# Optimization experiments

Measured on AMD Instinct MI355X. Metric: run time of the kernel, lower is better.

Reference implementation:

```python
import jax, jax.numpy as jnp
import numpy as np

B, T, CF, D, H, HD, L, HID = 32, 384, 128, 512, 16, 32, 16, 512
EPS = 1e-6

def _make_pe():
    pos = np.arange(T, dtype=np.float32)[:, None]
    div = np.exp(np.arange(0, D, 2, dtype=np.float32) * (-np.log(10000.0) / D))
    pe = np.zeros((T, D), dtype=np.float32)
    pe[:, 0::2] = np.sin(pos * div)
    pe[:, 1::2] = np.cos(pos * div)
    return jnp.asarray(pe)

def setup_inputs() -> dict:
    key = jax.random.key(0)
    ks = jax.random.split(key, 12)
    n = lambda k, shp: jax.random.normal(k, shp, dtype=jnp.float32) * 0.02
    return {
        "index": jax.random.normal(ks[0], (B, T, CF), dtype=jnp.float32),
        "targets": jax.random.normal(ks[1], (B, T, CF), dtype=jnp.float32),
        "W_embed": n(ks[2], (CF, D)), "b_embed": jnp.zeros((D,), jnp.float32),
        "pe": _make_pe(), "learnable_pe": jnp.zeros((T, D), jnp.float32),
        "Wq": n(ks[3], (L, H, D, HD)), "Wk": n(ks[4], (L, H, D, HD)), "Wv": n(ks[5], (L, H, D, HD)),
        "Wproj": n(ks[6], (L, D, D)), "bproj": jnp.zeros((L, D), jnp.float32),
        "ln1_g": jnp.ones((L, D), jnp.float32), "ln1_b": jnp.zeros((L, D), jnp.float32),
        "ln2_g": jnp.ones((L, D), jnp.float32), "ln2_b": jnp.zeros((L, D), jnp.float32),
        "W1": n(ks[7], (L, D, HID)), "b1": jnp.zeros((L, HID), jnp.float32),
        "W2": n(ks[8], (L, HID, D)), "b2": jnp.zeros((L, D), jnp.float32),
        "W_final": n(ks[9], (D, CF)), "b_final": jnp.zeros((CF,), jnp.float32),
    }

def _ln(x, g, b):
    m = jnp.mean(x, axis=-1, keepdims=True)
    v = jnp.mean(jnp.square(x - m), axis=-1, keepdims=True)
    return (x - m) / jnp.sqrt(v + EPS) * g + b

def reference(index, targets, W_embed, b_embed, pe, learnable_pe,
              Wq, Wk, Wv, Wproj, bproj, ln1_g, ln1_b, ln2_g, ln2_b,
              W1, b1, W2, b2, W_final, b_final):
    mask = jnp.tril(jnp.ones((T, T), dtype=bool))
    # NOTE: original scales by 1/sqrt(C) where C = n_embed (input dim), not head_size
    scale = 1.0 / jnp.sqrt(jnp.float32(D))
    x = index @ W_embed + b_embed          # [B,T,D]
    x = x + pe + learnable_pe

    def blk(x, p):
        wq, wk, wv, wp, bp, g1, bl1, g2, bl2, w1, bb1, w2, bb2 = p
        h = _ln(x, g1, bl1)
        q = jnp.einsum('btc,hcd->bhtd', h, wq)
        k = jnp.einsum('btc,hcd->bhtd', h, wk)
        v = jnp.einsum('btc,hcd->bhtd', h, wv)
        s = jnp.einsum('bhtd,bhsd->bhts', q, k) * scale   # [B,H,T,T]
        s = jnp.where(mask, s, -jnp.inf)
        w = jax.nn.softmax(s, axis=-1)
        o = jnp.einsum('bhts,bhsd->bhtd', w, v)
        o = o.transpose(0, 2, 1, 3).reshape(x.shape[0], T, H * HD)
        x = x + o @ wp + bp                                # attn residual (dropout=eval)
        h2 = _ln(x, g2, bl2)
        x = x + jax.nn.relu(h2 @ w1 + bb1) @ w2 + bb2      # FFN residual
        return x, None

    x, _ = jax.lax.scan(blk, x, (Wq, Wk, Wv, Wproj, bproj, ln1_g, ln1_b,
                                 ln2_g, ln2_b, W1, b1, W2, b2))
    logits = x @ W_final + b_final         # [B,T,CF]
    loss = jnp.mean(jnp.square(logits - targets))
    return logits, loss
```

## Files before the change

### kernel.cpp

```cpp
#include <hip/hip_runtime.h>
#include <hip/hip_bf16.h>

#define B_   32
#define T_   384
#define CF_  128
#define D_   512
#define H_   16
#define HD_  32
#define L_   16
#define HID_ 512
#define M_   (B_*T_)

typedef __bf16 bf16x8 __attribute__((ext_vector_type(8)));
typedef float  f32x4  __attribute__((ext_vector_type(4)));

__device__ __forceinline__ float bf2f(unsigned short u){
    unsigned int x = ((unsigned int)u) << 16;
    return __builtin_bit_cast(float, x);
}
__device__ __forceinline__ unsigned short f2bf(float f){
    unsigned int u = __builtin_bit_cast(unsigned int, f);
    u += 0x7FFFu + ((u >> 16) & 1u);
    return (unsigned short)(u >> 16);
}
__device__ __forceinline__ unsigned int cvtpk(float lo, float hi){
    unsigned int r;
    asm("v_cvt_pk_bf16_f32 %0, %1, %2" : "=v"(r) : "v"(lo), "v"(hi));
    return r;
}

typedef const __attribute__((address_space(1))) unsigned int* gas_p;
typedef __attribute__((address_space(3))) unsigned int*       las_p;
__device__ __forceinline__ void gload16(const void* g, void* l){
    __builtin_amdgcn_global_load_lds((gas_p)g, (las_p)l, 16, 0, 0);
}

#define QSCALE 0.06376580687097174f

template<int EPI>
__global__ __launch_bounds__(256) void gemm_k(
    const unsigned short* __restrict__ A,
    const unsigned short* __restrict__ Bt,
    const float* __restrict__ aux0,
    const float* __restrict__ aux1,
    const float* __restrict__ aux2,
    float* __restrict__ fout,
    unsigned short* __restrict__ bout,
    int K)
{
    __shared__ unsigned short lA[2][128*32];
    __shared__ unsigned short lB[2][128*32];

    const int tid  = threadIdx.x;
    const int lane = tid & 63;
    const int w    = tid >> 6;
    const int wm   = w >> 1, wn = w & 1;
    const int li   = lane & 15, ls = lane >> 4;
    const int m0   = blockIdx.x * 128;
    const int n0   = blockIdx.y * 128;
    const int nkt  = K >> 5;

    const int e0 = tid, e1 = tid + 256;
    const int r0 = e0 >> 2, s0 = (e0 & 3) ^ ((r0 >> 1) & 3);
    const int r1 = e1 >> 2, s1 = (e1 & 3) ^ ((r1 >> 1) & 3);
    const unsigned short* gA0 = A  + (size_t)(m0 + r0)*K + s0*8;
    const unsigned short* gA1 = A  + (size_t)(m0 + r1)*K + s1*8;
    const unsigned short* gB0 = Bt + (size_t)(n0 + r0)*K + s0*8;
    const unsigned short* gB1 = Bt + (size_t)(n0 + r1)*K + s1*8;

#define STAGE(c, kt) do{ \
    const int ko_ = (kt)*32; \
    gload16(gA0 + ko_, &lA[c][w*512]); \
    gload16(gA1 + ko_, &lA[c][2048 + w*512]); \
    gload16(gB0 + ko_, &lB[c][w*512]); \
    gload16(gB1 + ko_, &lB[c][2048 + w*512]); \
}while(0)

    f32x4 acc[4][4];
    #pragma unroll
    for (int i=0;i<4;i++)
        #pragma unroll
        for (int j=0;j<4;j++) acc[i][j] = (f32x4){0.f,0.f,0.f,0.f};

    STAGE(0, 0);
    asm volatile("s_waitcnt vmcnt(0)" ::: "memory");
    __syncthreads();

    int cur = 0;
    for (int kt = 0; kt < nkt; ++kt){
        if (kt + 1 < nkt) STAGE(cur^1, kt+1);
        bf16x8 af[4], bf[4];
        #pragma unroll
        for (int f=0; f<4; ++f){
            const int rA = wm*64 + f*16 + li;
            af[f] = *(const bf16x8*)&lA[cur][rA*32 + ((ls ^ ((rA>>1)&3))*8)];
            const int rB = wn*64 + f*16 + li;
            bf[f] = *(const bf16x8*)&lB[cur][rB*32 + ((ls ^ ((rB>>1)&3))*8)];
        }
        #pragma unroll
        for (int i=0;i<4;i++)
            #pragma unroll
            for (int j=0;j<4;j++)
                acc[i][j] = __builtin_amdgcn_mfma_f32_16x16x32_bf16(af[i], bf[j], acc[i][j], 0, 0, 0);
        __syncthreads();
        cur ^= 1;
    }
#undef STAGE

    #pragma unroll
    for (int i=0;i<4;i++){
        #pragma unroll
        for (int j=0;j<4;j++){
            #pragma unroll
            for (int t=0;t<4;t++){
                const int row = m0 + wm*64 + i*16 + ls*4 + t;
                const int col = n0 + wn*64 + j*16 + li;
                const float v = acc[i][j][t];
                if constexpr (EPI == 0){
                    const int tt = row % T_;
                    bout[row*D_ + col] = f2bf(v + aux0[col] + aux1[tt*D_ + col] + aux2[tt*D_ + col]);
                } else if constexpr (EPI == 2){
                    const int idx = row*D_ + col;
                    bout[idx] = f2bf(bf2f(bout[idx]) + v + aux0[col]);
                } else if constexpr (EPI == 3){
                    const float r = v + aux0[col];
                    bout[row*HID_ + col] = f2bf(r > 0.f ? r : 0.f);
                } else {
                    fout[row*CF_ + col] = v + aux0[col];
                }
            }
        }
    }
}

__global__ __launch_bounds__(256) void gemm192_k(
    const unsigned short* __restrict__ A,
    const unsigned short* __restrict__ Bt,
    unsigned short* __restrict__ bout,
    int K)
{
    __shared__ unsigned short lA[2][128*32];
    __shared__ unsigned short lB[2][192*32];

    const int tid  = threadIdx.x;
    const int lane = tid & 63;
    const int w    = tid >> 6;
    const int wm   = w >> 1, wn = w & 1;
    const int li   = lane & 15, ls = lane >> 4;
    const int m0   = blockIdx.x * 128;
    const int n0   = blockIdx.y * 192;
    const int nkt  = K >> 5;

    const int ea0 = tid, ea1 = tid + 256;
    const int ra0 = ea0 >> 2, sa0 = (ea0 & 3) ^ ((ra0 >> 1) & 3);
    const int ra1 = ea1 >> 2, sa1 = (ea1 & 3) ^ ((ra1 >> 1) & 3);
    const unsigned short* gA0 = A + (size_t)(m0 + ra0)*K + sa0*8;
    const unsigned short* gA1 = A + (size_t)(m0 + ra1)*K + sa1*8;

    const int eb0 = tid, eb1 = tid + 256, eb2 = tid + 512;
    const int rb0 = eb0 >> 2, sb0 = (eb0 & 3) ^ ((rb0 >> 1) & 3);
    const int rb1 = eb1 >> 2, sb1 = (eb1 & 3) ^ ((rb1 >> 1) & 3);
    const int rb2 = eb2 >> 2, sb2 = (eb2 & 3) ^ ((rb2 >> 1) & 3);
    const unsigned short* gB0 = Bt + (size_t)(n0 + rb0)*K + sb0*8;
    const unsigned short* gB1 = Bt + (size_t)(n0 + rb1)*K + sb1*8;
    const unsigned short* gB2 = Bt + (size_t)(n0 + rb2)*K + sb2*8;

#define STAGE192(c, kt) do{ \
    const int ko_ = (kt)*32; \
    gload16(gA0 + ko_, &lA[c][w*512]); \
    gload16(gA1 + ko_, &lA[c][2048 + w*512]); \
    gload16(gB0 + ko_, &lB[c][w*512]); \
    gload16(gB1 + ko_, &lB[c][2048 + w*512]); \
    gload16(gB2 + ko_, &lB[c][4096 + w*512]); \
}while(0)

    f32x4 acc[4][6];
    #pragma unroll
    for (int i=0;i<4;i++)
        #pragma unroll
        for (int j=0;j<6;j++) acc[i][j] = (f32x4){0.f,0.f,0.f,0.f};

    STAGE192(0, 0);
    asm volatile("s_waitcnt vmcnt(0)" ::: "memory");
    __syncthreads();

    int cur = 0;
    for (int kt = 0; kt < nkt; ++kt){
        if (kt + 1 < nkt) STAGE192(cur^1, kt+1);
        bf16x8 af[4], bf[6];
        #pragma unroll
        for (int f=0; f<4; ++f){
            const int rA = wm*64 + f*16 + li;
            af[f] = *(const bf16x8*)&lA[cur][rA*32 + ((ls ^ ((rA>>1)&3))*8)];
        }
        #pragma unroll
        for (int f=0; f<6; ++f){
            const int rB = wn*96 + f*16 + li;
            bf[f] = *(const bf16x8*)&lB[cur][rB*32 + ((ls ^ ((rB>>1)&3))*8)];
        }
        #pragma unroll
        for (int i=0;i<4;i++)
            #pragma unroll
            for (int j=0;j<6;j++)
                acc[i][j] = __builtin_amdgcn_mfma_f32_16x16x32_bf16(af[i], bf[j], acc[i][j], 0, 0, 0);
        __syncthreads();
        cur ^= 1;
    }
#undef STAGE192

    #pragma unroll
    for (int i=0;i<4;i++){
        #pragma unroll
        for (int j=0;j<6;j++){
            const int row0 = m0 + wm*64 + i*16 + ls*4;
            const int col  = n0 + wn*96 + j*16 + li;
            const int mat = col >> 9, nl = col & 511;
            const int hh = nl >> 5, dd = nl & 31;
            const int bb = row0 / T_, tt0 = row0 - bb*T_;
            if (mat == 2){
                alignas(8) unsigned short p4[4];
                #pragma unroll
                for (int t=0;t<4;t++) p4[t] = f2bf(acc[i][j][t]);
                *(uint2*)(bout + 2*(size_t)(M_*D_)
                          + ((size_t)(bb*H_ + hh)*HD_ + dd)*T_ + tt0) = *(const uint2*)p4;
            } else {
                #pragma unroll
                for (int t=0;t<4;t++){
                    float v = acc[i][j][t];
                    if (mat == 0) v *= QSCALE;
                    bout[(size_t)mat*(M_*D_)
                         + (((size_t)(bb*H_ + hh)*T_ + tt0 + t)*HD_) + dd] = f2bf(v);
                }
            }
        }
    }
}

__global__ __launch_bounds__(256) void ln_k(const unsigned short* __restrict__ x,
                                            const float* __restrict__ g,
                                            const float* __restrict__ b,
                                            unsigned short* __restrict__ out)
{
    const int w = threadIdx.x >> 6, lane = threadIdx.x & 63;
    const int row = blockIdx.x*4 + w;
    const unsigned short* xr = x + (size_t)row*D_ + lane*8;
    const uint4 raw = *(const uint4*)xr;
    const unsigned short* rs = (const unsigned short*)&raw;
    float v8[8];
    float s = 0.f, q2 = 0.f;
    #pragma unroll
    for (int i=0;i<8;i++){
        v8[i] = bf2f(rs[i]);
        s  += v8[i];
        q2 += v8[i]*v8[i];
    }
    #pragma unroll
    for (int off=32; off; off>>=1){
        s  += __shfl_xor(s,  off);
        q2 += __shfl_xor(q2, off);
    }
    const float mean = s * (1.f/512.f);
    const float var  = q2 * (1.f/512.f) - mean*mean;
    const float rstd = rsqrtf(var + 1e-6f);
    const float4 gA = *(const float4*)(g + lane*8);
    const float4 gB = *(const float4*)(g + lane*8 + 4);
    const float4 bA = *(const float4*)(b + lane*8);
    const float4 bB = *(const float4*)(b + lane*8 + 4);
    alignas(16) unsigned short o8[8];
    o8[0] = f2bf((v8[0]-mean)*rstd*gA.x + bA.x);
    o8[1] = f2bf((v8[1]-mean)*rstd*gA.y + bA.y);
    o8[2] = f2bf((v8[2]-mean)*rstd*gA.z + bA.z);
    o8[3] = f2bf((v8[3]-mean)*rstd*gA.w + bA.w);
    o8[4] = f2bf((v8[4]-mean)*rstd*gB.x + bB.x);
    o8[5] = f2bf((v8[5]-mean)*rstd*gB.y + bB.y);
    o8[6] = f2bf((v8[6]-mean)*rstd*gB.z + bB.z);
    o8[7] = f2bf((v8[7]-mean)*rstd*gB.w + bB.w);
    *(uint4*)(out + (size_t)row*D_ + lane*8) = *(const uint4*)o8;
}

__global__ __launch_bounds__(256) void attn_k(const unsigned short* __restrict__ q,
                                              const unsigned short* __restrict__ k,
                                              const unsigned short* __restrict__ vt,
                                              unsigned short* __restrict__ o)
{
    __shared__ unsigned int Pb[4][2*16*18];

    const int orig = blockIdx.x;
    const int wg   = (orig & 7)*192 + (orig >> 3);
    const int bh   = wg / 3;
    const int t0   = (wg - bh*3) * 128;

    const int tid  = threadIdx.x;
    const int lane = tid & 63, w = tid >> 6;
    const int li   = lane & 15, ls = lane >> 4;
    const unsigned short* qb = q  + (size_t)bh*(T_*HD_);
    const unsigned short* kb = k  + (size_t)bh*(T_*HD_);
    const unsigned short* vb = vt + (size_t)bh*(HD_*T_);

    const int trow0 = t0 + w*32;
    const bf16x8 qaA = *(const bf16x8*)(qb + (trow0 + li)*HD_ + ls*8);
    const bf16x8 qaB = *(const bf16x8*)(qb + (trow0 + 16 + li)*HD_ + ls*8);
    const int nfull = trow0 >> 5;

    float lsA = 0.f, lsB = 0.f;
    f32x4 oA0={0.f,0.f,0.f,0.f}, oA1={0.f,0.f,0.f,0.f};
    f32x4 oB0={0.f,0.f,0.f,0.f}, oB1={0.f,0.f,0.f,0.f};
    unsigned int* pwA = Pb[w];
    unsigned int* pwB = Pb[w] + 288;

    bf16x8 kf0 = *(const bf16x8*)(kb + li*HD_ + ls*8);
    bf16x8 kf1 = *(const bf16x8*)(kb + (16 + li)*HD_ + ls*8);
    bf16x8 vf0 = *(const bf16x8*)(vb + li*T_ + ls*8);
    bf16x8 vf1 = *(const bf16x8*)(vb + (16 + li)*T_ + ls*8);

    for (int c = 0; c < nfull; ++c){
        f32x4 sA0={0.f,0.f,0.f,0.f}, sA1={0.f,0.f,0.f,0.f};
        f32x4 sB0={0.f,0.f,0.f,0.f}, sB1={0.f,0.f,0.f,0.f};
        sA0 = __builtin_amdgcn_mfma_f32_16x16x32_bf16(kf0, qaA, sA0, 0, 0, 0);
        sA1 = __builtin_amdgcn_mfma_f32_16x16x32_bf16(kf1, qaA, sA1, 0, 0, 0);
        sB0 = __builtin_amdgcn_mfma_f32_16x16x32_bf16(kf0, qaB, sB0, 0, 0, 0);
        sB1 = __builtin_amdgcn_mfma_f32_16x16x32_bf16(kf1, qaB, sB1, 0, 0, 0);
        kf0 = *(const bf16x8*)(kb + ((c+1)*32 + li)*HD_ + ls*8);
        kf1 = *(const bf16x8*)(kb + ((c+1)*32 + 16 + li)*HD_ + ls*8);

        float pA0[4], pA1[4], pB0[4], pB1[4];
        #pragma unroll
        for (int j=0;j<4;j++){
            pA0[j] = exp2f(sA0[j]); pA1[j] = exp2f(sA1[j]);
            pB0[j] = exp2f(sB0[j]); pB1[j] = exp2f(sB1[j]);
        }
        lsA += pA0[0]+pA0[1]+pA0[2]+pA0[3]+pA1[0]+pA1[1]+pA1[2]+pA1[3];
        lsB += pB0[0]+pB0[1]+pB0[2]+pB0[3]+pB1[0]+pB1[1]+pB1[2]+pB1[3];

        const uint2 wA0 = { cvtpk(pA0[0], pA0[1]), cvtpk(pA0[2], pA0[3]) };
        const uint2 wA1 = { cvtpk(pA1[0], pA1[1]), cvtpk(pA1[2], pA1[3]) };
        const uint2 wB0 = { cvtpk(pB0[0], pB0[1]), cvtpk(pB0[2], pB0[3]) };
        const uint2 wB1 = { cvtpk(pB1[0], pB1[1]), cvtpk(pB1[2], pB1[3]) };
        *(uint2*)&pwA[li*18 + ls*2]     = wA0;
        *(uint2*)&pwA[li*18 + 8 + ls*2] = wA1;
        *(uint2*)&pwB[li*18 + ls*2]     = wB0;
        *(uint2*)&pwB[li*18 + 8 + ls*2] = wB1;
        asm volatile("s_waitcnt lgkmcnt(0)" ::: "memory");
        const bf16x8 paA = *(const bf16x8*)&pwA[li*18 + ls*4];
        const bf16x8 paB = *(const bf16x8*)&pwB[li*18 + ls*4];

        oA0 = __builtin_amdgcn_mfma_f32_16x16x32_bf16(paA, vf0, oA0, 0, 0, 0);
        oA1 = __builtin_amdgcn_mfma_f32_16x16x32_bf16(paA, vf1, oA1, 0, 0, 0);
        oB0 = __builtin_amdgcn_mfma_f32_16x16x32_bf16(paB, vf0, oB0, 0, 0, 0);
        oB1 = __builtin_amdgcn_mfma_f32_16x16x32_bf16(paB, vf1, oB1, 0, 0, 0);
        vf0 = *(const bf16x8*)(vb + li*T_ + (c+1)*32 + ls*8);
        vf1 = *(const bf16x8*)(vb + (16 + li)*T_ + (c+1)*32 + ls*8);
    }

    {
        f32x4 sA0={0.f,0.f,0.f,0.f}, sB0={0.f,0.f,0.f,0.f}, sB1={0.f,0.f,0.f,0.f};
        sA0 = __builtin_amdgcn_mfma_f32_16x16x32_bf16(kf0, qaA, sA0, 0, 0, 0);
        sB0 = __builtin_amdgcn_mfma_f32_16x16x32_bf16(kf0, qaB, sB0, 0, 0, 0);
        sB1 = __builtin_amdgcn_mfma_f32_16x16x32_bf16(kf1, qaB, sB1, 0, 0, 0);

        const int qA = li, qB = 16 + li;
        float pA0[4], pB0[4], pB1[4];
        #pragma unroll
        for (int j=0;j<4;j++){
            const int k0 = ls*4 + j;
            pA0[j] = (k0 <= qA)      ? exp2f(sA0[j]) : 0.f;
            pB0[j] = exp2f(sB0[j]);
            pB1[j] = (k0 + 16 <= qB) ? exp2f(sB1[j]) : 0.f;
        }
        lsA += pA0[0]+pA0[1]+pA0[2]+pA0[3];
        lsB += pB0[0]+pB0[1]+pB0[2]+pB0[3]+pB1[0]+pB1[1]+pB1[2]+pB1[3];

        const uint2 wA0 = { cvtpk(pA0[0], pA0[1]), cvtpk(pA0[2], pA0[3]) };
        const uint2 wB0 = { cvtpk(pB0[0], pB0[1]), cvtpk(pB0[2], pB0[3]) };
        const uint2 wB1 = { cvtpk(pB1[0], pB1[1]), cvtpk(pB1[2], pB1[3]) };
        const uint2 zz  = { 0u, 0u };
        *(uint2*)&pwA[li*18 + ls*2]     = wA0;
        *(uint2*)&pwA[li*18 + 8 + ls*2] = zz;
        *(uint2*)&pwB[li*18 + ls*2]     = wB0;
        *(uint2*)&pwB[li*18 + 8 + ls*2] = wB1;
        asm volatile("s_waitcnt lgkmcnt(0)" ::: "memory");
        const bf16x8 paA = *(const bf16x8*)&pwA[li*18 + ls*4];
        const bf16x8 paB = *(const bf16x8*)&pwB[li*18 + ls*4];

        oA0 = __builtin_amdgcn_mfma_f32_16x16x32_bf16(paA, vf0, oA0, 0, 0, 0);
        oA1 = __builtin_amdgcn_mfma_f32_16x16x32_bf16(paA, vf1, oA1, 0, 0, 0);
        oB0 = __builtin_amdgcn_mfma_f32_16x16x32_bf16(paB, vf0, oB0, 0, 0, 0);
        oB1 = __builtin_amdgcn_mfma_f32_16x16x32_bf16(paB, vf1, oB1, 0, 0, 0);
    }

    lsA += __shfl_xor(lsA, 16);  lsA += __shfl_xor(lsA, 32);
    lsB += __shfl_xor(lsB, 16);  lsB += __shfl_xor(lsB, 32);

    const int bb = bh >> 4, hh = bh & 15;
    #pragma unroll
    for (int j=0;j<4;j++){
        const float rsA = __shfl(lsA, ls*4 + j);
        const float rsB = __shfl(lsB, ls*4 + j);
        const float iA = 1.f / rsA, iB = 1.f / rsB;
        const int tgA = trow0 + ls*4 + j;
        const int tgB = tgA + 16;
        o[(size_t)(bb*T_ + tgA)*D_ + hh*HD_ + li]      = f2bf(oA0[j]*iA);
        o[(size_t)(bb*T_ + tgA)*D_ + hh*HD_ + 16 + li] = f2bf(oA1[j]*iA);
        o[(size_t)(bb*T_ + tgB)*D_ + hh*HD_ + li]      = f2bf(oB0[j]*iB);
        o[(size_t)(bb*T_ + tgB)*D_ + hh*HD_ + 16 + li] = f2bf(oB1[j]*iB);
    }
}

__global__ __launch_bounds__(256) void packT_k(const float* __restrict__ src,
                                               unsigned short* __restrict__ dst,
                                               int R, int C)
{
    __shared__ unsigned short tile[64][72];
    const int z  = blockIdx.z;
    const float* s = src + (size_t)z*R*C;
    unsigned short* d = dst + (size_t)z*R*C;
    const int c0 = blockIdx.x*64, r0 = blockIdx.y*64;

    for (int it = threadIdx.x; it < 1024; it += 256){
        const int rr  = it >> 4;
        const int cc4 = (it & 15) << 2;
        const float4 v = *(const float4*)(s + (size_t)(r0+rr)*C + c0 + cc4);
        tile[cc4  ][rr] = f2bf(v.x);
        tile[cc4+1][rr] = f2bf(v.y);
        tile[cc4+2][rr] = f2bf(v.z);
        tile[cc4+3][rr] = f2bf(v.w);
    }
    __syncthreads();
    for (int it = threadIdx.x; it < 512; it += 256){
        const int cc = it >> 3;
        const int ch = (it & 7) << 3;
        *(uint4*)(d + (size_t)(c0+cc)*R + r0 + ch) = *(const uint4*)&tile[cc][ch];
    }
}

__global__ __launch_bounds__(256) void pack_qkv_k(const float* __restrict__ Wq,
                                                  const float* __restrict__ Wk,
                                                  const float* __restrict__ Wv,
                                                  unsigned short* __restrict__ dst)
{
    __shared__ unsigned short tile[32][136];
    const int kc  = blockIdx.x;
    const int mat = blockIdx.y >> 4;
    const int h   = blockIdx.y & 15;
    const int l   = blockIdx.z;
    const float* src = ((mat==0) ? Wq : (mat==1) ? Wk : Wv)
                     + ((size_t)(l*H_ + h)*D_ + kc*128)*HD_;

    for (int it = threadIdx.x; it < 1024; it += 256){
        const int rr  = it >> 3;
        const int dd4 = (it & 7) << 2;
        const float4 v = *(const float4*)(src + (size_t)rr*HD_ + dd4);
        tile[dd4  ][rr] = f2bf(v.x);
        tile[dd4+1][rr] = f2bf(v.y);
        tile[dd4+2][rr] = f2bf(v.z);
        tile[dd4+3][rr] = f2bf(v.w);
    }
    __syncthreads();
    unsigned short* dp = dst + (size_t)l*786432 + (size_t)mat*262144 + kc*128;
    for (int it = threadIdx.x; it < 512; it += 256){
        const int dd = it >> 4;
        const int ch = (it & 15) << 3;
        *(uint4*)(dp + (size_t)(h*32 + dd)*512 + ch) = *(const uint4*)&tile[dd][ch];
    }
}

__global__ void cast4_k(const float* __restrict__ src, unsigned short* __restrict__ dst, int total4)
{
    const int i = blockIdx.x*256 + threadIdx.x;
    if (i >= total4) return;
    const float4 vv = ((const float4*)src)[i];
    alignas(8) unsigned short t[4] = { f2bf(vv.x), f2bf(vv.y), f2bf(vv.z), f2bf(vv.w) };
    *(uint2*)(dst + (size_t)i*4) = *(const uint2*)t;
}

__global__ __launch_bounds__(256) void loss1_k(const float* __restrict__ logits,
                                               const float* __restrict__ tgt,
                                               float* __restrict__ part)
{
    float s = 0.f;
    for (int i = blockIdx.x*256 + threadIdx.x; i < M_*CF_; i += 256*1024){
        const float d = logits[i] - tgt[i];
        s += d*d;
    }
    #pragma unroll
    for (int off=32; off; off>>=1) s += __shfl_xor(s, off);
    __shared__ float ws4[4];
    if ((threadIdx.x & 63) == 0) ws4[threadIdx.x >> 6] = s;
    __syncthreads();
    if (threadIdx.x == 0) part[blockIdx.x] = ws4[0]+ws4[1]+ws4[2]+ws4[3];
}

__global__ __launch_bounds__(256) void loss2_k(const float* __restrict__ part,
                                               float* __restrict__ out)
{
    float s = 0.f;
    for (int i = threadIdx.x; i < 1024; i += 256) s += part[i];
    #pragma unroll
    for (int off=32; off; off>>=1) s += __shfl_xor(s, off);
    __shared__ float ws4[4];
    if ((threadIdx.x & 63) == 0) ws4[threadIdx.x >> 6] = s;
    __syncthreads();
    if (threadIdx.x == 0) out[0] = (ws4[0]+ws4[1]+ws4[2]+ws4[3]) * (1.f/(float)(M_*CF_));
}

static constexpr size_t X_OFF     = 0;
static constexpr size_t H_OFF     = 25165824;
static constexpr size_t O_OFF     = 37748736;
static constexpr size_t QKV_OFF   = 50331648;
static constexpr size_t WQKV_OFF  = 88080384;
static constexpr size_t WPROJ_OFF = 113246208;
static constexpr size_t W1_OFF    = 121634816;
static constexpr size_t W2_OFF    = 130023424;
static constexpr size_t WEMB_OFF  = 138412032;
static constexpr size_t WFIN_OFF  = 138543104;
static constexpr size_t PART_OFF  = 138674176;

extern "C" void kernel_launch(void* const* d_in, const int* in_sizes, int n_in,
                              void* d_out, int out_size, void* d_ws, size_t ws_size,
                              hipStream_t stream)
{
    const float* index   = (const float*)d_in[0];
    const float* targets = (const float*)d_in[1];
    const float* W_embed = (const float*)d_in[2];
    const float* b_embed = (const float*)d_in[3];
    const float* pe      = (const float*)d_in[4];
    const float* lpe     = (const float*)d_in[5];
    const float* Wq      = (const float*)d_in[6];
    const float* Wk      = (const float*)d_in[7];
    const float* Wv      = (const float*)d_in[8];
    const float* Wproj   = (const float*)d_in[9];
    const float* bproj   = (const float*)d_in[10];
    const float* ln1g    = (const float*)d_in[11];
    const float* ln1b    = (const float*)d_in[12];
    const float* ln2g    = (const float*)d_in[13];
    const float* ln2b    = (const float*)d_in[14];
    const float* W1      = (const float*)d_in[15];
    const float* b1      = (const float*)d_in[16];
    const float* W2      = (const float*)d_in[17];
    const float* b2      = (const float*)d_in[18];
    const float* Wfin    = (const float*)d_in[19];
    const float* bfin    = (const float*)d_in[20];

    char* ws = (char*)d_ws;
    unsigned short* xb    = (unsigned short*)(ws + X_OFF);
    unsigned short* hbuf  = (unsigned short*)(ws + H_OFF);
    unsigned short* obuf  = (unsigned short*)(ws + O_OFF);
    unsigned short* qkv   = (unsigned short*)(ws + QKV_OFF);
    unsigned short* wqkvp = (unsigned short*)(ws + WQKV_OFF);
    unsigned short* wprojp= (unsigned short*)(ws + WPROJ_OFF);
    unsigned short* w1p   = (unsigned short*)(ws + W1_OFF);
    unsigned short* w2p   = (unsigned short*)(ws + W2_OFF);
    unsigned short* wembp = (unsigned short*)(ws + WEMB_OFF);
    unsigned short* wfinp = (unsigned short*)(ws + WFIN_OFF);
    float*          part  = (float*)(ws + PART_OFF);
    float*          logits= (float*)d_out;

    pack_qkv_k<<<dim3(4,48,16), 256, 0, stream>>>(Wq, Wk, Wv, wqkvp);
    packT_k<<<dim3(8,8,16), 256, 0, stream>>>(Wproj, wprojp, 512, 512);
    packT_k<<<dim3(8,8,16), 256, 0, stream>>>(W1,    w1p,    512, 512);
    packT_k<<<dim3(8,8,16), 256, 0, stream>>>(W2,    w2p,    512, 512);
    packT_k<<<dim3(8,2,1),  256, 0, stream>>>(W_embed, wembp, 128, 512);
    packT_k<<<dim3(2,8,1),  256, 0, stream>>>(Wfin,    wfinp, 512, 128);

    cast4_k<<<1536, 256, 0, stream>>>(index, obuf, 393216);
    gemm_k<0><<<dim3(96,4), 256, 0, stream>>>(obuf, wembp, b_embed, pe, lpe, nullptr, xb, 128);

    for (int l = 0; l < L_; ++l){
        ln_k<<<3072, 256, 0, stream>>>(xb, ln1g + l*512, ln1b + l*512, hbuf);
        gemm192_k<<<dim3(96,8), 256, 0, stream>>>(hbuf, wqkvp + (size_t)l*786432, qkv, 512);
        attn_k<<<1536, 256, 0, stream>>>(qkv, qkv + 6291456, qkv + 2*6291456, obuf);
        gemm_k<2><<<dim3(96,4), 256, 0, stream>>>(obuf, wprojp + (size_t)l*262144,
                                                  bproj + l*512, nullptr, nullptr, nullptr, xb, 512);
        ln_k<<<3072, 256, 0, stream>>>(xb, ln2g + l*512, ln2b + l*512, hbuf);
        gemm_k<3><<<dim3(96,4), 256, 0, stream>>>(hbuf, w1p + (size_t)l*262144,
                                                  b1 + l*512, nullptr, nullptr, nullptr, obuf, 512);
        gemm_k<2><<<dim3(96,4), 256, 0, stream>>>(obuf, w2p + (size_t)l*262144,
                                                  b2 + l*512, nullptr, nullptr, nullptr, xb, 512);
    }

    gemm_k<4><<<dim3(96,1), 256, 0, stream>>>(xb, wfinp, bfin, nullptr, nullptr, logits, nullptr, 512);
    loss1_k<<<1024, 256, 0, stream>>>(logits, targets, part);
    loss2_k<<<1, 256, 0, stream>>>(part, logits + 1572864);
}
```

Before: 1.877 ms.

## Process 64 query rows per wave in attention to reuse K/V fragments

The attention kernel now runs 2 waves per block, each handling 64 query rows (four 16-row groups) instead of 32. Each K and V fragment loaded from global memory therefore feeds twice as many MFMAs, and the diagonal handling is split into two masked tail steps. The cost is more registers per wave and larger per-wave LDS staging. Causal work is also less balanced, since waves whose rows lie further down the sequence run longer loops.

```diff
diff --git a/kernel.cpp b/kernel.cpp
--- a/kernel.cpp
+++ b/kernel.cpp
@@ -278,12 +278,12 @@
     *(uint4*)(out + (size_t)row*D_ + lane*8) = *(const uint4*)o8;
 }
 
-__global__ __launch_bounds__(256) void attn_k(const unsigned short* __restrict__ q,
+__global__ __launch_bounds__(128) void attn_k(const unsigned short* __restrict__ q,
                                               const unsigned short* __restrict__ k,
                                               const unsigned short* __restrict__ vt,
                                               unsigned short* __restrict__ o)
 {
-    __shared__ unsigned int Pb[4][2*16*18];
+    __shared__ unsigned int Pb[2][4*288];
 
     const int orig = blockIdx.x;
     const int wg   = (orig & 7)*192 + (orig >> 3);
@@ -297,16 +297,22 @@
     const unsigned short* kb = k  + (size_t)bh*(T_*HD_);
     const unsigned short* vb = vt + (size_t)bh*(HD_*T_);
 
-    const int trow0 = t0 + w*32;
-    const bf16x8 qaA = *(const bf16x8*)(qb + (trow0 + li)*HD_ + ls*8);
+    const int trow0 = t0 + w*64;
+    const bf16x8 qaA = *(const bf16x8*)(qb + (trow0 +      li)*HD_ + ls*8);
     const bf16x8 qaB = *(const bf16x8*)(qb + (trow0 + 16 + li)*HD_ + ls*8);
+    const bf16x8 qaC = *(const bf16x8*)(qb + (trow0 + 32 + li)*HD_ + ls*8);
+    const bf16x8 qaD = *(const bf16x8*)(qb + (trow0 + 48 + li)*HD_ + ls*8);
     const int nfull = trow0 >> 5;
 
-    float lsA = 0.f, lsB = 0.f;
+    float lsA = 0.f, lsB = 0.f, lsC = 0.f, lsD = 0.f;
     f32x4 oA0={0.f,0.f,0.f,0.f}, oA1={0.f,0.f,0.f,0.f};
     f32x4 oB0={0.f,0.f,0.f,0.f}, oB1={0.f,0.f,0.f,0.f};
+    f32x4 oC0={0.f,0.f,0.f,0.f}, oC1={0.f,0.f,0.f,0.f};
+    f32x4 oD0={0.f,0.f,0.f,0.f}, oD1={0.f,0.f,0.f,0.f};
     unsigned int* pwA = Pb[w];
     unsigned int* pwB = Pb[w] + 288;
+    unsigned int* pwC = Pb[w] + 576;
+    unsigned int* pwD = Pb[w] + 864;
 
     bf16x8 kf0 = *(const bf16x8*)(kb + li*HD_ + ls*8);
     bf16x8 kf1 = *(const bf16x8*)(kb + (16 + li)*HD_ + ls*8);
@@ -316,93 +322,188 @@
     for (int c = 0; c < nfull; ++c){
         f32x4 sA0={0.f,0.f,0.f,0.f}, sA1={0.f,0.f,0.f,0.f};
         f32x4 sB0={0.f,0.f,0.f,0.f}, sB1={0.f,0.f,0.f,0.f};
+        f32x4 sC0={0.f,0.f,0.f,0.f}, sC1={0.f,0.f,0.f,0.f};
+        f32x4 sD0={0.f,0.f,0.f,0.f}, sD1={0.f,0.f,0.f,0.f};
         sA0 = __builtin_amdgcn_mfma_f32_16x16x32_bf16(kf0, qaA, sA0, 0, 0, 0);
         sA1 = __builtin_amdgcn_mfma_f32_16x16x32_bf16(kf1, qaA, sA1, 0, 0, 0);
         sB0 = __builtin_amdgcn_mfma_f32_16x16x32_bf16(kf0, qaB, sB0, 0, 0, 0);
         sB1 = __builtin_amdgcn_mfma_f32_16x16x32_bf16(kf1, qaB, sB1, 0, 0, 0);
+        sC0 = __builtin_amdgcn_mfma_f32_16x16x32_bf16(kf0, qaC, sC0, 0, 0, 0);
+        sC1 = __builtin_amdgcn_mfma_f32_16x16x32_bf16(kf1, qaC, sC1, 0, 0, 0);
+        sD0 = __builtin_amdgcn_mfma_f32_16x16x32_bf16(kf0, qaD, sD0, 0, 0, 0);
+        sD1 = __builtin_amdgcn_mfma_f32_16x16x32_bf16(kf1, qaD, sD1, 0, 0, 0);
         kf0 = *(const bf16x8*)(kb + ((c+1)*32 + li)*HD_ + ls*8);
         kf1 = *(const bf16x8*)(kb + ((c+1)*32 + 16 + li)*HD_ + ls*8);
 
-        float pA0[4], pA1[4], pB0[4], pB1[4];
+        float pA0[4], pA1[4], pB0[4], pB1[4], pC0[4], pC1[4], pD0[4], pD1[4];
         #pragma unroll
         for (int j=0;j<4;j++){
             pA0[j] = exp2f(sA0[j]); pA1[j] = exp2f(sA1[j]);
             pB0[j] = exp2f(sB0[j]); pB1[j] = exp2f(sB1[j]);
+            pC0[j] = exp2f(sC0[j]); pC1[j] = exp2f(sC1[j]);
+            pD0[j] = exp2f(sD0[j]); pD1[j] = exp2f(sD1[j]);
         }
         lsA += pA0[0]+pA0[1]+pA0[2]+pA0[3]+pA1[0]+pA1[1]+pA1[2]+pA1[3];
         lsB += pB0[0]+pB0[1]+pB0[2]+pB0[3]+pB1[0]+pB1[1]+pB1[2]+pB1[3];
+        lsC += pC0[0]+pC0[1]+pC0[2]+pC0[3]+pC1[0]+pC1[1]+pC1[2]+pC1[3];
+        lsD += pD0[0]+pD0[1]+pD0[2]+pD0[3]+pD1[0]+pD1[1]+pD1[2]+pD1[3];
 
         const uint2 wA0 = { cvtpk(pA0[0], pA0[1]), cvtpk(pA0[2], pA0[3]) };
         const uint2 wA1 = { cvtpk(pA1[0], pA1[1]), cvtpk(pA1[2], pA1[3]) };
         const uint2 wB0 = { cvtpk(pB0[0], pB0[1]), cvtpk(pB0[2], pB0[3]) };
         const uint2 wB1 = { cvtpk(pB1[0], pB1[1]), cvtpk(pB1[2], pB1[3]) };
+        const uint2 wC0 = { cvtpk(pC0[0], pC0[1]), cvtpk(pC0[2], pC0[3]) };
+        const uint2 wC1 = { cvtpk(pC1[0], pC1[1]), cvtpk(pC1[2], pC1[3]) };
+        const uint2 wD0 = { cvtpk(pD0[0], pD0[1]), cvtpk(pD0[2], pD0[3]) };
+        const uint2 wD1 = { cvtpk(pD1[0], pD1[1]), cvtpk(pD1[2], pD1[3]) };
         *(uint2*)&pwA[li*18 + ls*2]     = wA0;
         *(uint2*)&pwA[li*18 + 8 + ls*2] = wA1;
         *(uint2*)&pwB[li*18 + ls*2]     = wB0;
         *(uint2*)&pwB[li*18 + 8 + ls*2] = wB1;
+        *(uint2*)&pwC[li*18 + ls*2]     = wC0;
+        *(uint2*)&pwC[li*18 + 8 + ls*2] = wC1;
+        *(uint2*)&pwD[li*18 + ls*2]     = wD0;
+        *(uint2*)&pwD[li*18 + 8 + ls*2] = wD1;
         asm volatile("s_waitcnt lgkmcnt(0)" ::: "memory");
         const bf16x8 paA = *(const bf16x8*)&pwA[li*18 + ls*4];
         const bf16x8 paB = *(const bf16x8*)&pwB[li*18 + ls*4];
+        const bf16x8 paC = *(const bf16x8*)&pwC[li*18 + ls*4];
+        const bf16x8 paD = *(const bf16x8*)&pwD[li*18 + ls*4];
 
         oA0 = __builtin_amdgcn_mfma_f32_16x16x32_bf16(paA, vf0, oA0, 0, 0, 0);
         oA1 = __builtin_amdgcn_mfma_f32_16x16x32_bf16(paA, vf1, oA1, 0, 0, 0);
         oB0 = __builtin_amdgcn_mfma_f32_16x16x32_bf16(paB, vf0, oB0, 0, 0, 0);
         oB1 = __builtin_amdgcn_mfma_f32_16x16x32_bf16(paB, vf1, oB1, 0, 0, 0);
+        oC0 = __builtin_amdgcn_mfma_f32_16x16x32_bf16(paC, vf0, oC0, 0, 0, 0);
+        oC1 = __builtin_amdgcn_mfma_f32_16x16x32_bf16(paC, vf1, oC1, 0, 0, 0);
+        oD0 = __builtin_amdgcn_mfma_f32_16x16x32_bf16(paD, vf0, oD0, 0, 0, 0);
+        oD1 = __builtin_amdgcn_mfma_f32_16x16x32_bf16(paD, vf1, oD1, 0, 0, 0);
         vf0 = *(const bf16x8*)(vb + li*T_ + (c+1)*32 + ls*8);
         vf1 = *(const bf16x8*)(vb + (16 + li)*T_ + (c+1)*32 + ls*8);
     }
 
     {
-        f32x4 sA0={0.f,0.f,0.f,0.f}, sB0={0.f,0.f,0.f,0.f}, sB1={0.f,0.f,0.f,0.f};
+        f32x4 sA0={0.f,0.f,0.f,0.f};
+        f32x4 sB0={0.f,0.f,0.f,0.f}, sB1={0.f,0.f,0.f,0.f};
+        f32x4 sC0={0.f,0.f,0.f,0.f}, sC1={0.f,0.f,0.f,0.f};
+        f32x4 sD0={0.f,0.f,0.f,0.f}, sD1={0.f,0.f,0.f,0.f};
         sA0 = __builtin_amdgcn_mfma_f32_16x16x32_bf16(kf0, qaA, sA0, 0, 0, 0);
         sB0 = __builtin_amdgcn_mfma_f32_16x16x32_bf16(kf0, qaB, sB0, 0, 0, 0);
         sB1 = __builtin_amdgcn_mfma_f32_16x16x32_bf16(kf1, qaB, sB1, 0, 0, 0);
-
-        const int qA = li, qB = 16 + li;
-        float pA0[4], pB0[4], pB1[4];
+        sC0 = __builtin_amdgcn_mfma_f32_16x16x32_bf16(kf0, qaC, sC0, 0, 0, 0);
+        sC1 = __builtin_amdgcn_mfma_f32_16x16x32_bf16(kf1, qaC, sC1, 0, 0, 0);
+        sD0 = __builtin_amdgcn_mfma_f32_16x16x32_bf16(kf0, qaD, sD0, 0, 0, 0);
+        sD1 = __builtin_amdgcn_mfma_f32_16x16x32_bf16(kf1, qaD, sD1, 0, 0, 0);
+        kf0 = *(const bf16x8*)(kb + (trow0 + 32 + li)*HD_ + ls*8);
+        kf1 = *(const bf16x8*)(kb + (trow0 + 48 + li)*HD_ + ls*8);
+
+        float pA0[4], pB0[4], pB1[4], pC0[4], pC1[4], pD0[4], pD1[4];
         #pragma unroll
         for (int j=0;j<4;j++){
             const int k0 = ls*4 + j;
-            pA0[j] = (k0 <= qA)      ? exp2f(sA0[j]) : 0.f;
+            pA0[j] = (k0 <= li) ? exp2f(sA0[j]) : 0.f;
             pB0[j] = exp2f(sB0[j]);
-            pB1[j] = (k0 + 16 <= qB) ? exp2f(sB1[j]) : 0.f;
+            pB1[j] = (k0 <= li) ? exp2f(sB1[j]) : 0.f;
+            pC0[j] = exp2f(sC0[j]); pC1[j] = exp2f(sC1[j]);
+            pD0[j] = exp2f(sD0[j]); pD1[j] = exp2f(sD1[j]);
         }
         lsA += pA0[0]+pA0[1]+pA0[2]+pA0[3];
         lsB += pB0[0]+pB0[1]+pB0[2]+pB0[3]+pB1[0]+pB1[1]+pB1[2]+pB1[3];
-
+        lsC += pC0[0]+pC0[1]+pC0[2]+pC0[3]+pC1[0]+pC1[1]+pC1[2]+pC1[3];
+        lsD += pD0[0]+pD0[1]+pD0[2]+pD0[3]+pD1[0]+pD1[1]+pD1[2]+pD1[3];
+
+        const uint2 zz = { 0u, 0u };
         const uint2 wA0 = { cvtpk(pA0[0], pA0[1]), cvtpk(pA0[2], pA0[3]) };
         const uint2 wB0 = { cvtpk(pB0[0], pB0[1]), cvtpk(pB0[2], pB0[3]) };
         const uint2 wB1 = { cvtpk(pB1[0], pB1[1]), cvtpk(pB1[2], pB1[3]) };
-        const uint2 zz  = { 0u, 0u };
+        const uint2 wC0 = { cvtpk(pC0[0], pC0[1]), cvtpk(pC0[2], pC0[3]) };
+        const uint2 wC1 = { cvtpk(pC1[0], pC1[1]), cvtpk(pC1[2], pC1[3]) };
+        const uint2 wD0 = { cvtpk(pD0[0], pD0[1]), cvtpk(pD0[2], pD0[3]) };
+        const uint2 wD1 = { cvtpk(pD1[0], pD1[1]), cvtpk(pD1[2], pD1[3]) };
         *(uint2*)&pwA[li*18 + ls*2]     = wA0;
         *(uint2*)&pwA[li*18 + 8 + ls*2] = zz;
         *(uint2*)&pwB[li*18 + ls*2]     = wB0;
         *(uint2*)&pwB[li*18 + 8 + ls*2] = wB1;
+        *(uint2*)&pwC[li*18 + ls*2]     = wC0;
+        *(uint2*)&pwC[li*18 + 8 + ls*2] = wC1;
+        *(uint2*)&pwD[li*18 + ls*2]     = wD0;
+        *(uint2*)&pwD[li*18 + 8 + ls*2] = wD1;
         asm volatile("s_waitcnt lgkmcnt(0)" ::: "memory");
         const bf16x8 paA = *(const bf16x8*)&pwA[li*18 + ls*4];
         const bf16x8 paB = *(const bf16x8*)&pwB[li*18 + ls*4];
+        const bf16x8 paC = *(const bf16x8*)&pwC[li*18 + ls*4];
+        const bf16x8 paD = *(const bf16x8*)&pwD[li*18 + ls*4];
 
         oA0 = __builtin_amdgcn_mfma_f32_16x16x32_bf16(paA, vf0, oA0, 0, 0, 0);
         oA1 = __builtin_amdgcn_mfma_f32_16x16x32_bf16(paA, vf1, oA1, 0, 0, 0);
         oB0 = __builtin_amdgcn_mfma_f32_16x16x32_bf16(paB, vf0, oB0, 0, 0, 0);
         oB1 = __builtin_amdgcn_mfma_f32_16x16x32_bf16(paB, vf1, oB1, 0, 0, 0);
+        oC0 = __builtin_amdgcn_mfma_f32_16x16x32_bf16(paC, vf0, oC0, 0, 0, 0);
+        oC1 = __builtin_amdgcn_mfma_f32_16x16x32_bf16(paC, vf1, oC1, 0, 0, 0);
+        oD0 = __builtin_amdgcn_mfma_f32_16x16x32_bf16(paD, vf0, oD0, 0, 0, 0);
+        oD1 = __builtin_amdgcn_mfma_f32_16x16x32_bf16(paD, vf1, oD1, 0, 0, 0);
+        vf0 = *(const bf16x8*)(vb + li*T_ + trow0 + 32 + ls*8);
+        vf1 = *(const bf16x8*)(vb + (16 + li)*T_ + trow0 + 32 + ls*8);
+    }
+
+    {
+        f32x4 sC0={0.f,0.f,0.f,0.f};
+        f32x4 sD0={0.f,0.f,0.f,0.f}, sD1={0.f,0.f,0.f,0.f};
+        sC0 = __builtin_amdgcn_mfma_f32_16x16x32_bf16(kf0, qaC, sC0, 0, 0, 0);
+        sD0 = __builtin_amdgcn_mfma_f32_16x16x32_bf16(kf0, qaD, sD0, 0, 0, 0);
+        sD1 = __builtin_amdgcn_mfma_f32_16x16x32_bf16(kf1, qaD, sD1, 0, 0, 0);
+
+        float pC0[4], pD0[4], pD1[4];
+        #pragma unroll
+        for (int j=0;j<4;j++){
+            const int k0 = ls*4 + j;
+            pC0[j] = (k0 <= li) ? exp2f(sC0[j]) : 0.f;
+            pD0[j] = exp2f(sD0[j]);
+            pD1[j] = (k0 <= li) ? exp2f(sD1[j]) : 0.f;
+        }
+        lsC += pC0[0]+pC0[1]+pC0[2]+pC0[3];
+        lsD += pD0[0]+pD0[1]+pD0[2]+pD0[3]+pD1[0]+pD1[1]+pD1[2]+pD1[3];
+
+        const uint2 zz = { 0u, 0u };
+        const uint2 wC0 = { cvtpk(pC0[0], pC0[1]), cvtpk(pC0[2], pC0[3]) };
+        const uint2 wD0 = { cvtpk(pD0[0], pD0[1]), cvtpk(pD0[2], pD0[3]) };
+        const uint2 wD1 = { cvtpk(pD1[0], pD1[1]), cvtpk(pD1[2], pD1[3]) };
+        *(uint2*)&pwC[li*18 + ls*2]     = wC0;
+        *(uint2*)&pwC[li*18 + 8 + ls*2] = zz;
+        *(uint2*)&pwD[li*18 + ls*2]     = wD0;
+        *(uint2*)&pwD[li*18 + 8 + ls*2] = wD1;
+        asm volatile("s_waitcnt lgkmcnt(0)" ::: "memory");
+        const bf16x8 paC = *(const bf16x8*)&pwC[li*18 + ls*4];
+        const bf16x8 paD = *(const bf16x8*)&pwD[li*18 + ls*4];
+
+        oC0 = __builtin_amdgcn_mfma_f32_16x16x32_bf16(paC, vf0, oC0, 0, 0, 0);
+        oC1 = __builtin_amdgcn_mfma_f32_16x16x32_bf16(paC, vf1, oC1, 0, 0, 0);
+        oD0 = __builtin_amdgcn_mfma_f32_16x16x32_bf16(paD, vf0, oD0, 0, 0, 0);
+        oD1 = __builtin_amdgcn_mfma_f32_16x16x32_bf16(paD, vf1, oD1, 0, 0, 0);
     }
 
     lsA += __shfl_xor(lsA, 16);  lsA += __shfl_xor(lsA, 32);
     lsB += __shfl_xor(lsB, 16);  lsB += __shfl_xor(lsB, 32);
+    lsC += __shfl_xor(lsC, 16);  lsC += __shfl_xor(lsC, 32);
+    lsD += __shfl_xor(lsD, 16);  lsD += __shfl_xor(lsD, 32);
 
     const int bb = bh >> 4, hh = bh & 15;
     #pragma unroll
     for (int j=0;j<4;j++){
-        const float rsA = __shfl(lsA, ls*4 + j);
-        const float rsB = __shfl(lsB, ls*4 + j);
-        const float iA = 1.f / rsA, iB = 1.f / rsB;
-        const int tgA = trow0 + ls*4 + j;
-        const int tgB = tgA + 16;
-        o[(size_t)(bb*T_ + tgA)*D_ + hh*HD_ + li]      = f2bf(oA0[j]*iA);
-        o[(size_t)(bb*T_ + tgA)*D_ + hh*HD_ + 16 + li] = f2bf(oA1[j]*iA);
-        o[(size_t)(bb*T_ + tgB)*D_ + hh*HD_ + li]      = f2bf(oB0[j]*iB);
-        o[(size_t)(bb*T_ + tgB)*D_ + hh*HD_ + 16 + li] = f2bf(oB1[j]*iB);
+        const int rl = ls*4 + j;
+        const float iA = 1.f / __shfl(lsA, rl);
+        const float iB = 1.f / __shfl(lsB, rl);
+        const float iC = 1.f / __shfl(lsC, rl);
+        const float iD = 1.f / __shfl(lsD, rl);
+        const int tgA = trow0 + rl;
+        o[(size_t)(bb*T_ + tgA)*D_ + hh*HD_ + li]           = f2bf(oA0[j]*iA);
+        o[(size_t)(bb*T_ + tgA)*D_ + hh*HD_ + 16 + li]      = f2bf(oA1[j]*iA);
+        o[(size_t)(bb*T_ + tgA + 16)*D_ + hh*HD_ + li]      = f2bf(oB0[j]*iB);
+        o[(size_t)(bb*T_ + tgA + 16)*D_ + hh*HD_ + 16 + li] = f2bf(oB1[j]*iB);
+        o[(size_t)(bb*T_ + tgA + 32)*D_ + hh*HD_ + li]      = f2bf(oC0[j]*iC);
+        o[(size_t)(bb*T_ + tgA + 32)*D_ + hh*HD_ + 16 + li] = f2bf(oC1[j]*iC);
+        o[(size_t)(bb*T_ + tgA + 48)*D_ + hh*HD_ + li]      = f2bf(oD0[j]*iD);
+        o[(size_t)(bb*T_ + tgA + 48)*D_ + hh*HD_ + 16 + li] = f2bf(oD1[j]*iD);
     }
 }
 
@@ -568,7 +669,7 @@
     for (int l = 0; l < L_; ++l){
         ln_k<<<3072, 256, 0, stream>>>(xb, ln1g + l*512, ln1b + l*512, hbuf);
         gemm192_k<<<dim3(96,8), 256, 0, stream>>>(hbuf, wqkvp + (size_t)l*786432, qkv, 512);
-        attn_k<<<1536, 256, 0, stream>>>(qkv, qkv + 6291456, qkv + 2*6291456, obuf);
+        attn_k<<<1536, 128, 0, stream>>>(qkv, qkv + 6291456, qkv + 2*6291456, obuf);
         gemm_k<2><<<dim3(96,4), 256, 0, stream>>>(obuf, wprojp + (size_t)l*262144,
                                                   bproj + l*512, nullptr, nullptr, nullptr, xb, 512);
         ln_k<<<3072, 256, 0, stream>>>(xb, ln2g + l*512, ln2b + l*512, hbuf);
```

Measured after the change: 1.899 ms. Within noise of the previous version (+1.1%).
